# Kernel optimization log

Hardware: AMD Instinct MI355X
Metric: run time of the kernel (lower is better)

Reference implementation:

```python
import jax, jax.numpy as jnp
import numpy as np


def setup_inputs() -> dict:
    key = jax.random.key(0)
    ks = jax.random.split(key, 4)
    B, L, E = 2, 2048, 512
    scale = 0.02
    return {
        "x": jax.random.normal(ks[0], (B, L, E), dtype=jnp.float32),
        "Wq": jax.random.normal(ks[1], (E, E), dtype=jnp.float32) * scale,
        "bq": jnp.zeros((E,), dtype=jnp.float32),
        "Wk": jax.random.normal(ks[2], (E, E), dtype=jnp.float32) * scale,
        "bk": jnp.zeros((E,), dtype=jnp.float32),
        "Wv": jax.random.normal(ks[3], (E, E), dtype=jnp.float32) * scale,
        "bv": jnp.zeros((E,), dtype=jnp.float32),
        "window_size": 64,
    }


def reference(x, Wq, bq, Wk, bk, Wv, bv, window_size):
    # x: [B, L, E]; Linear weights stored torch-style as [out, in].
    B, L, E = x.shape
    q = jnp.einsum("ble,fe->blf", x, Wq) + bq  # [B, L, E]
    k = jnp.einsum("ble,fe->blf", x, Wk) + bk
    v = jnp.einsum("ble,fe->blf", x, Wv) + bv

    w = window_size
    W = 2 * w + 1
    # Window indices per query position i: [i-w, i+w], clipped; invalid masked.
    offsets = jnp.arange(-w, w + 1)                 # [W]
    idx = jnp.arange(L)[:, None] + offsets[None, :]  # [L, W]
    valid = (idx >= 0) & (idx < L)                   # [L, W]
    idx_c = jnp.clip(idx, 0, L - 1)

    k_win = k[:, idx_c]  # [B, L, W, E]
    v_win = v[:, idx_c]  # [B, L, W, E]

    scores = jnp.einsum("ble,blwe->blw", q, k_win) / jnp.sqrt(jnp.float32(E))
    scores = jnp.where(valid[None, :, :], scores, -jnp.inf)
    probs = jax.nn.softmax(scores, axis=-1)          # [B, L, W]
    out = jnp.einsum("blw,blwe->ble", probs, v_win)  # [B, L, E]
    return out
```

## Files before the change

### kernel.cpp

```cpp
#include <hip/hip_runtime.h>
#include <cstdint>
#include <cstddef>

#define L_SEQ 2048
#define E_DIM 512
#define B_SZ 2
#define WIN 64
#define SCALE_QK 0.044194173824159216f

typedef __attribute__((ext_vector_type(8))) short short8;
typedef __attribute__((ext_vector_type(4))) float floatx4;

__device__ __forceinline__ unsigned short f2bf(float f) {
    unsigned int u = __float_as_uint(f);
    u += 0x7FFFu + ((u >> 16) & 1u);
    return (unsigned short)(u >> 16);
}

__global__ __launch_bounds__(256) void cvt_kernel(
    const float* __restrict__ x, const float* __restrict__ wq,
    const float* __restrict__ wk, const float* __restrict__ wv,
    unsigned short* __restrict__ xb, unsigned short* __restrict__ wb)
{
    long i = (long)blockIdx.x * 256 + threadIdx.x;
    const float* src;
    unsigned short* dst;
    long off;
    if (i < 524288) {
        src = x; dst = xb; off = i;
    } else {
        long j = i - 524288;
        int w = (int)(j >> 16);
        off = j & 65535;
        src = (w == 0) ? wq : ((w == 1) ? wk : wv);
        dst = wb + (long)w * 262144;
    }
    float4 f = ((const float4*)src)[off];
    ushort4 o;
    o.x = f2bf(f.x); o.y = f2bf(f.y); o.z = f2bf(f.z); o.w = f2bf(f.w);
    ((ushort4*)dst)[off] = o;
}

#define BLD 40
#define TLD 136
__global__ __launch_bounds__(256) void qkv_gemm(
    const unsigned short* __restrict__ xb,
    const unsigned short* __restrict__ wb,
    const float* __restrict__ bq, const float* __restrict__ bk, const float* __restrict__ bv,
    unsigned short* __restrict__ q, unsigned short* __restrict__ k,
    unsigned short* __restrict__ vt)
{
    __shared__ __align__(16) char smem[35840];
    unsigned short* As = (unsigned short*)smem;
    unsigned short* Bs = (unsigned short*)(smem + 10240);
    unsigned short* Tl = (unsigned short*)smem;

    const int t = threadIdx.x;
    const int w = t >> 6, l = t & 63;
    const int m0 = blockIdx.x * 128, n0 = blockIdx.y * 128, z = blockIdx.z;
    const unsigned short* W = wb + (size_t)z * 262144;
    const float* bias = (z == 0) ? bq : ((z == 1) ? bk : bv);

    floatx4 acc[4][4] = {};
    const int wm = (w >> 1) * 64, wn = (w & 1) * 64;
    const int fr = l & 15, fq = l >> 4, fk = fq * 8;

    const int srow = t >> 2, scol = (t & 3) * 8;

    for (int kk = 0; kk < 512; kk += 32) {
#pragma unroll
        for (int s = 0; s < 2; s++) {
            int row = srow + s * 64;
            *(uint4*)&As[row * BLD + scol] = *(const uint4*)&xb[(size_t)(m0 + row) * 512 + kk + scol];
            *(uint4*)&Bs[row * BLD + scol] = *(const uint4*)&W [(size_t)(n0 + row) * 512 + kk + scol];
        }
        __syncthreads();
        short8 a[4], b[4];
#pragma unroll
        for (int i = 0; i < 4; i++) a[i] = *(const short8*)&As[(wm + i * 16 + fr) * BLD + fk];
#pragma unroll
        for (int j = 0; j < 4; j++) b[j] = *(const short8*)&Bs[(wn + j * 16 + fr) * BLD + fk];
#pragma unroll
        for (int i = 0; i < 4; i++)
#pragma unroll
            for (int j = 0; j < 4; j++)
                acc[i][j] = __builtin_amdgcn_mfma_f32_16x16x32_bf16(a[i], b[j], acc[i][j], 0, 0, 0);
        __syncthreads();
    }

    float bv_[4];
#pragma unroll
    for (int j = 0; j < 4; j++) bv_[j] = bias[n0 + wn + j * 16 + fr];

    if (z < 2) {
#pragma unroll
        for (int i = 0; i < 4; i++)
#pragma unroll
            for (int j = 0; j < 4; j++)
#pragma unroll
                for (int r = 0; r < 4; r++)
                    Tl[(wm + i * 16 + fq * 4 + r) * TLD + wn + j * 16 + fr] =
                        f2bf(acc[i][j][r] + bv_[j]);
    } else {
#pragma unroll
        for (int i = 0; i < 4; i++)
#pragma unroll
            for (int j = 0; j < 4; j++)
#pragma unroll
                for (int r = 0; r < 4; r++)
                    Tl[(wn + j * 16 + fr) * TLD + wm + i * 16 + fq * 4 + r] =
                        f2bf(acc[i][j][r] + bv_[j]);
    }
    __syncthreads();

    const int tl = t >> 1;
    unsigned short* out = (z == 0) ? q : ((z == 1) ? k : vt);
#pragma unroll
    for (int s = 0; s < 8; s++) {
        int c = (t & 1) * 64 + s * 8;
        uint4 val = *(const uint4*)&Tl[tl * TLD + c];
        if (z < 2)
            *(uint4*)&out[(size_t)(m0 + tl) * 512 + n0 + c] = val;
        else
            *(uint4*)&out[(size_t)(n0 + tl) * 4096 + m0 + c] = val;
    }
}

__global__ __launch_bounds__(64) void scores_kernel(
    const unsigned short* __restrict__ qb, const unsigned short* __restrict__ kb,
    float* __restrict__ S)
{
    const int l = threadIdx.x;
    const int fr = l & 15, fq = l >> 4;
    const int Q0 = blockIdx.x * 16;
    const int nt = blockIdx.y;
    const int b  = blockIdx.z;
    const int R0 = Q0 - WIN;
    const int tok = R0 + nt * 16 + fr;
    const bool kvalid = (tok >= 0) && (tok < L_SEQ);

    const unsigned short* qrow = qb + (size_t)(b * L_SEQ + Q0 + fr) * 512 + fq * 8;
    const unsigned short* krow = kb + (size_t)(b * L_SEQ) * 512 + (size_t)tok * 512 + fq * 8;

    floatx4 acc = {};
#pragma unroll
    for (int ks = 0; ks < 16; ks++) {
        short8 a = *(const short8*)(qrow + ks * 32);
        short8 bfr = {};
        if (kvalid) bfr = *(const short8*)(krow + ks * 32);
        acc = __builtin_amdgcn_mfma_f32_16x16x32_bf16(a, bfr, acc, 0, 0, 0);
    }

    const int jg = nt * 16 + fr;
    float* Srow = S + (size_t)(b * L_SEQ + Q0) * 160 + jg;
#pragma unroll
    for (int r = 0; r < 4; r++) {
        int qq = fq * 4 + r;
        bool valid = (jg >= qq) && (jg <= qq + 128) && kvalid;
        Srow[(size_t)qq * 160] = valid ? acc[r] * SCALE_QK : -1e30f;
    }
}

__global__ __launch_bounds__(256) void softmax_kernel(
    const float* __restrict__ S, unsigned short* __restrict__ P)
{
    const int t = threadIdx.x;
    const int row = blockIdx.x * 4 + (t >> 6);
    const int l = t & 63;
    const float* Sr = S + (size_t)row * 160;
    float s1 = Sr[l], s2 = Sr[64 + l];
    float s3 = (l < 16) ? Sr[128 + l] : -1e30f;
    float m = fmaxf(fmaxf(s1, s2), s3);
#pragma unroll
    for (int d = 32; d >= 1; d >>= 1) m = fmaxf(m, __shfl_xor(m, d));
    float e1 = __expf(s1 - m), e2 = __expf(s2 - m);
    float e3 = (l < 16) ? __expf(s3 - m) : 0.f;
    float sum = e1 + e2 + e3;
#pragma unroll
    for (int d = 32; d >= 1; d >>= 1) sum += __shfl_xor(sum, d);
    float inv = 1.f / sum;
    unsigned short* Pr = P + (size_t)row * 160;
    Pr[l] = f2bf(e1 * inv);
    Pr[64 + l] = f2bf(e2 * inv);
    if (l < 16) Pr[128 + l] = f2bf(e3 * inv);
    else if (l < 32) Pr[128 + l] = 0;
}

__global__ __launch_bounds__(64) void pv_kernel(
    const unsigned short* __restrict__ P, const unsigned short* __restrict__ vt,
    float* __restrict__ out)
{
    const int l = threadIdx.x;
    const int fr = l & 15, fq = l >> 4;
    const int Q0 = blockIdx.x * 16;
    const int EC = blockIdx.y * 32;
    const int b  = blockIdx.z;
    const int R0 = Q0 - WIN;

    const unsigned short* Prow = P + (size_t)(b * L_SEQ + Q0 + fr) * 160 + fq * 8;

    floatx4 oa[2] = {};
#pragma unroll
    for (int ks = 0; ks < 5; ks++) {
        short8 a = *(const short8*)(Prow + ks * 32);
        int tok0 = R0 + ks * 32 + fq * 8;
        bool tv = (tok0 >= 0) && (tok0 < L_SEQ);
#pragma unroll
        for (int et = 0; et < 2; et++) {
            short8 bfr = {};
            if (tv) bfr = *(const short8*)&vt[(size_t)(EC + et * 16 + fr) * 4096 + b * L_SEQ + tok0];
            oa[et] = __builtin_amdgcn_mfma_f32_16x16x32_bf16(a, bfr, oa[et], 0, 0, 0);
        }
    }

    float* op = out + (size_t)b * L_SEQ * E_DIM;
#pragma unroll
    for (int et = 0; et < 2; et++)
#pragma unroll
        for (int r = 0; r < 4; r++)
            op[(size_t)(Q0 + fq * 4 + r) * 512 + EC + et * 16 + fr] = oa[et][r];
}

extern "C" void kernel_launch(void* const* d_in, const int* in_sizes, int n_in,
                              void* d_out, int out_size, void* d_ws, size_t ws_size,
                              hipStream_t stream)
{
    const float* x  = (const float*)d_in[0];
    const float* Wq = (const float*)d_in[1];
    const float* bq = (const float*)d_in[2];
    const float* Wk = (const float*)d_in[3];
    const float* bk = (const float*)d_in[4];
    const float* Wv = (const float*)d_in[5];
    const float* bv = (const float*)d_in[6];
    float* out = (float*)d_out;

    char* ws = (char*)d_ws;
    unsigned short* qb = (unsigned short*)(ws);
    unsigned short* kb = (unsigned short*)(ws + 4194304);
    unsigned short* vt = (unsigned short*)(ws + 8388608);
    unsigned short* xb = (unsigned short*)(ws + 12582912);
    unsigned short* wb = (unsigned short*)(ws + 16777216);
    float*          S  = (float*)(ws + 18350080);
    unsigned short* P  = (unsigned short*)(ws + 20971520);

    cvt_kernel<<<2816, 256, 0, stream>>>(x, Wq, Wk, Wv, xb, wb);
    qkv_gemm<<<dim3(32, 4, 3), 256, 0, stream>>>(xb, wb, bq, bk, bv, qb, kb, vt);
    scores_kernel<<<dim3(128, 9, 2), 64, 0, stream>>>(qb, kb, S);
    softmax_kernel<<<1024, 256, 0, stream>>>(S, P);
    pv_kernel<<<dim3(128, 16, 2), 64, 0, stream>>>(P, vt, out);
}
```

Baseline: 117.3 us.

## Fuse softmax into PV kernel and retile QKV GEMM with register prefetch

Removes the standalone softmax kernel; each PV block now loads its rows of fp32 scores, computes max and sum with cross-lane shuffles, and builds bf16 probabilities in registers before the MFMAs. The QKV GEMM switches to 64x64 tiles with a K-step of 64 and prefetches the next global tile into registers while computing, giving 1536 blocks instead of 384 for better occupancy on the CUs. The cost is that softmax work is now repeated by each of the 16 E-chunk blocks that share a query tile, and the smaller GEMM tiles reuse less data.

```diff
diff --git a/kernel.cpp b/kernel.cpp
--- a/kernel.cpp
+++ b/kernel.cpp
@@ -41,8 +41,7 @@
     ((ushort4*)dst)[off] = o;
 }
 
-#define BLD 40
-#define TLD 136
+#define ALD 72
 __global__ __launch_bounds__(256) void qkv_gemm(
     const unsigned short* __restrict__ xb,
     const unsigned short* __restrict__ wb,
@@ -50,79 +49,94 @@
     unsigned short* __restrict__ q, unsigned short* __restrict__ k,
     unsigned short* __restrict__ vt)
 {
-    __shared__ __align__(16) char smem[35840];
-    unsigned short* As = (unsigned short*)smem;
-    unsigned short* Bs = (unsigned short*)(smem + 10240);
-    unsigned short* Tl = (unsigned short*)smem;
+    __shared__ __align__(16) unsigned short As[64 * ALD];
+    __shared__ __align__(16) unsigned short Bs[64 * ALD];
 
     const int t = threadIdx.x;
     const int w = t >> 6, l = t & 63;
-    const int m0 = blockIdx.x * 128, n0 = blockIdx.y * 128, z = blockIdx.z;
+    const int m0 = blockIdx.x * 64, n0 = blockIdx.y * 64, z = blockIdx.z;
     const unsigned short* W = wb + (size_t)z * 262144;
     const float* bias = (z == 0) ? bq : ((z == 1) ? bk : bv);
 
-    floatx4 acc[4][4] = {};
-    const int wm = (w >> 1) * 64, wn = (w & 1) * 64;
+    floatx4 acc[2][2] = {};
+    const int wm = (w >> 1) * 32, wn = (w & 1) * 32;
     const int fr = l & 15, fq = l >> 4, fk = fq * 8;
 
-    const int srow = t >> 2, scol = (t & 3) * 8;
-
-    for (int kk = 0; kk < 512; kk += 32) {
-#pragma unroll
-        for (int s = 0; s < 2; s++) {
-            int row = srow + s * 64;
-            *(uint4*)&As[row * BLD + scol] = *(const uint4*)&xb[(size_t)(m0 + row) * 512 + kk + scol];
-            *(uint4*)&Bs[row * BLD + scol] = *(const uint4*)&W [(size_t)(n0 + row) * 512 + kk + scol];
+    const int srow = t >> 2, scol = (t & 3) * 16;
+    const unsigned short* gA = xb + (size_t)(m0 + srow) * 512 + scol;
+    const unsigned short* gB = W  + (size_t)(n0 + srow) * 512 + scol;
+
+    uint4 ra0 = *(const uint4*)(gA);     uint4 ra1 = *(const uint4*)(gA + 8);
+    uint4 rb0 = *(const uint4*)(gB);     uint4 rb1 = *(const uint4*)(gB + 8);
+
+    for (int it = 0; it < 8; it++) {
+        *(uint4*)&As[srow * ALD + scol]     = ra0;
+        *(uint4*)&As[srow * ALD + scol + 8] = ra1;
+        *(uint4*)&Bs[srow * ALD + scol]     = rb0;
+        *(uint4*)&Bs[srow * ALD + scol + 8] = rb1;
+        __syncthreads();
+        if (it < 7) {
+            int kk = (it + 1) * 64;
+            ra0 = *(const uint4*)(gA + kk); ra1 = *(const uint4*)(gA + kk + 8);
+            rb0 = *(const uint4*)(gB + kk); rb1 = *(const uint4*)(gB + kk + 8);
         }
+        short8 a[2][2], bf[2][2];
+#pragma unroll
+        for (int i = 0; i < 2; i++)
+#pragma unroll
+            for (int kh = 0; kh < 2; kh++)
+                a[i][kh] = *(const short8*)&As[(wm + i * 16 + fr) * ALD + kh * 32 + fk];
+#pragma unroll
+        for (int j = 0; j < 2; j++)
+#pragma unroll
+            for (int kh = 0; kh < 2; kh++)
+                bf[j][kh] = *(const short8*)&Bs[(wn + j * 16 + fr) * ALD + kh * 32 + fk];
+#pragma unroll
+        for (int kh = 0; kh < 2; kh++)
+#pragma unroll
+            for (int i = 0; i < 2; i++)
+#pragma unroll
+                for (int j = 0; j < 2; j++)
+                    acc[i][j] = __builtin_amdgcn_mfma_f32_16x16x32_bf16(a[i][kh], bf[j][kh], acc[i][j], 0, 0, 0);
         __syncthreads();
-        short8 a[4], b[4];
-#pragma unroll
-        for (int i = 0; i < 4; i++) a[i] = *(const short8*)&As[(wm + i * 16 + fr) * BLD + fk];
-#pragma unroll
-        for (int j = 0; j < 4; j++) b[j] = *(const short8*)&Bs[(wn + j * 16 + fr) * BLD + fk];
-#pragma unroll
-        for (int i = 0; i < 4; i++)
-#pragma unroll
-            for (int j = 0; j < 4; j++)
-                acc[i][j] = __builtin_amdgcn_mfma_f32_16x16x32_bf16(a[i], b[j], acc[i][j], 0, 0, 0);
-        __syncthreads();
-    }
-
-    float bv_[4];
-#pragma unroll
-    for (int j = 0; j < 4; j++) bv_[j] = bias[n0 + wn + j * 16 + fr];
+    }
+
+    unsigned short* Tl = As;
+    float bv_[2];
+#pragma unroll
+    for (int j = 0; j < 2; j++) bv_[j] = bias[n0 + wn + j * 16 + fr];
 
     if (z < 2) {
 #pragma unroll
-        for (int i = 0; i < 4; i++)
-#pragma unroll
-            for (int j = 0; j < 4; j++)
+        for (int i = 0; i < 2; i++)
+#pragma unroll
+            for (int j = 0; j < 2; j++)
 #pragma unroll
                 for (int r = 0; r < 4; r++)
-                    Tl[(wm + i * 16 + fq * 4 + r) * TLD + wn + j * 16 + fr] =
+                    Tl[(wm + i * 16 + fq * 4 + r) * ALD + wn + j * 16 + fr] =
                         f2bf(acc[i][j][r] + bv_[j]);
     } else {
 #pragma unroll
-        for (int i = 0; i < 4; i++)
-#pragma unroll
-            for (int j = 0; j < 4; j++)
+        for (int i = 0; i < 2; i++)
+#pragma unroll
+            for (int j = 0; j < 2; j++)
 #pragma unroll
                 for (int r = 0; r < 4; r++)
-                    Tl[(wn + j * 16 + fr) * TLD + wm + i * 16 + fq * 4 + r] =
+                    Tl[(wn + j * 16 + fr) * ALD + wm + i * 16 + fq * 4 + r] =
                         f2bf(acc[i][j][r] + bv_[j]);
     }
     __syncthreads();
 
-    const int tl = t >> 1;
-    unsigned short* out = (z == 0) ? q : ((z == 1) ? k : vt);
-#pragma unroll
-    for (int s = 0; s < 8; s++) {
-        int c = (t & 1) * 64 + s * 8;
-        uint4 val = *(const uint4*)&Tl[tl * TLD + c];
-        if (z < 2)
-            *(uint4*)&out[(size_t)(m0 + tl) * 512 + n0 + c] = val;
-        else
-            *(uint4*)&out[(size_t)(n0 + tl) * 4096 + m0 + c] = val;
+    const int tr = t >> 2, tc = (t & 3) * 16;
+    uint4 v0 = *(const uint4*)&Tl[tr * ALD + tc];
+    uint4 v1 = *(const uint4*)&Tl[tr * ALD + tc + 8];
+    if (z < 2) {
+        unsigned short* out = (z == 0) ? q : k;
+        *(uint4*)&out[(size_t)(m0 + tr) * 512 + n0 + tc]     = v0;
+        *(uint4*)&out[(size_t)(m0 + tr) * 512 + n0 + tc + 8] = v1;
+    } else {
+        *(uint4*)&vt[(size_t)(n0 + tr) * 4096 + m0 + tc]     = v0;
+        *(uint4*)&vt[(size_t)(n0 + tr) * 4096 + m0 + tc + 8] = v1;
     }
 }
 
@@ -161,33 +175,8 @@
     }
 }
 
-__global__ __launch_bounds__(256) void softmax_kernel(
-    const float* __restrict__ S, unsigned short* __restrict__ P)
-{
-    const int t = threadIdx.x;
-    const int row = blockIdx.x * 4 + (t >> 6);
-    const int l = t & 63;
-    const float* Sr = S + (size_t)row * 160;
-    float s1 = Sr[l], s2 = Sr[64 + l];
-    float s3 = (l < 16) ? Sr[128 + l] : -1e30f;
-    float m = fmaxf(fmaxf(s1, s2), s3);
-#pragma unroll
-    for (int d = 32; d >= 1; d >>= 1) m = fmaxf(m, __shfl_xor(m, d));
-    float e1 = __expf(s1 - m), e2 = __expf(s2 - m);
-    float e3 = (l < 16) ? __expf(s3 - m) : 0.f;
-    float sum = e1 + e2 + e3;
-#pragma unroll
-    for (int d = 32; d >= 1; d >>= 1) sum += __shfl_xor(sum, d);
-    float inv = 1.f / sum;
-    unsigned short* Pr = P + (size_t)row * 160;
-    Pr[l] = f2bf(e1 * inv);
-    Pr[64 + l] = f2bf(e2 * inv);
-    if (l < 16) Pr[128 + l] = f2bf(e3 * inv);
-    else if (l < 32) Pr[128 + l] = 0;
-}
-
 __global__ __launch_bounds__(64) void pv_kernel(
-    const unsigned short* __restrict__ P, const unsigned short* __restrict__ vt,
+    const float* __restrict__ S, const unsigned short* __restrict__ vt,
     float* __restrict__ out)
 {
     const int l = threadIdx.x;
@@ -197,19 +186,51 @@
     const int b  = blockIdx.z;
     const int R0 = Q0 - WIN;
 
-    const unsigned short* Prow = P + (size_t)(b * L_SEQ + Q0 + fr) * 160 + fq * 8;
+    const float* Srow = S + (size_t)(b * L_SEQ + Q0 + fr) * 160 + fq * 8;
+    float sv[5][8];
+#pragma unroll
+    for (int ks = 0; ks < 5; ks++) {
+        float4 u0 = *(const float4*)(Srow + ks * 32);
+        float4 u1 = *(const float4*)(Srow + ks * 32 + 4);
+        sv[ks][0] = u0.x; sv[ks][1] = u0.y; sv[ks][2] = u0.z; sv[ks][3] = u0.w;
+        sv[ks][4] = u1.x; sv[ks][5] = u1.y; sv[ks][6] = u1.z; sv[ks][7] = u1.w;
+    }
+    if (fq >= 2) {
+#pragma unroll
+        for (int j = 0; j < 8; j++) sv[4][j] = -1e30f;
+    }
+    float m = -1e30f;
+#pragma unroll
+    for (int ks = 0; ks < 5; ks++)
+#pragma unroll
+        for (int j = 0; j < 8; j++) m = fmaxf(m, sv[ks][j]);
+    m = fmaxf(m, __shfl_xor(m, 16));
+    m = fmaxf(m, __shfl_xor(m, 32));
+    float sum = 0.f;
+#pragma unroll
+    for (int ks = 0; ks < 5; ks++)
+#pragma unroll
+        for (int j = 0; j < 8; j++) { float e = __expf(sv[ks][j] - m); sv[ks][j] = e; sum += e; }
+    sum += __shfl_xor(sum, 16);
+    sum += __shfl_xor(sum, 32);
+    float inv = 1.f / sum;
+
+    short8 a[5];
+#pragma unroll
+    for (int ks = 0; ks < 5; ks++)
+#pragma unroll
+        for (int j = 0; j < 8; j++) a[ks][j] = (short)f2bf(sv[ks][j] * inv);
 
     floatx4 oa[2] = {};
 #pragma unroll
     for (int ks = 0; ks < 5; ks++) {
-        short8 a = *(const short8*)(Prow + ks * 32);
         int tok0 = R0 + ks * 32 + fq * 8;
         bool tv = (tok0 >= 0) && (tok0 < L_SEQ);
 #pragma unroll
         for (int et = 0; et < 2; et++) {
             short8 bfr = {};
             if (tv) bfr = *(const short8*)&vt[(size_t)(EC + et * 16 + fr) * 4096 + b * L_SEQ + tok0];
-            oa[et] = __builtin_amdgcn_mfma_f32_16x16x32_bf16(a, bfr, oa[et], 0, 0, 0);
+            oa[et] = __builtin_amdgcn_mfma_f32_16x16x32_bf16(a[ks], bfr, oa[et], 0, 0, 0);
         }
     }
 
@@ -241,11 +262,9 @@
     unsigned short* xb = (unsigned short*)(ws + 12582912);
     unsigned short* wb = (unsigned short*)(ws + 16777216);
     float*          S  = (float*)(ws + 18350080);
-    unsigned short* P  = (unsigned short*)(ws + 20971520);
 
     cvt_kernel<<<2816, 256, 0, stream>>>(x, Wq, Wk, Wv, xb, wb);
-    qkv_gemm<<<dim3(32, 4, 3), 256, 0, stream>>>(xb, wb, bq, bk, bv, qb, kb, vt);
+    qkv_gemm<<<dim3(64, 8, 3), 256, 0, stream>>>(xb, wb, bq, bk, bv, qb, kb, vt);
     scores_kernel<<<dim3(128, 9, 2), 64, 0, stream>>>(qb, kb, S);
-    softmax_kernel<<<1024, 256, 0, stream>>>(S, P);
-    pv_kernel<<<dim3(128, 16, 2), 64, 0, stream>>>(P, vt, out);
-}
+    pv_kernel<<<dim3(128, 16, 2), 64, 0, stream>>>(S, vt, out);
+}
```

Result: faster. 112.0 us (-4.5%).
